# Kernel tuning notes

Hardware: AMD Instinct MI355X
Metric: run time of the kernel (lower is better)

The kernel has to match this reference:

```python
import jax, jax.numpy as jnp
import numpy as np

N_NODES = 50000
N_EDGES = 800000
N_FEAT = 128
HIDDEN = 128
N_CLASSES = 10
N_GRAPHS = 100


def setup_inputs() -> dict:
    key = jax.random.key(0)
    ks = jax.random.split(key, 16)
    x = jax.random.normal(ks[0], (N_NODES, N_FEAT), dtype=jnp.float32)
    edge_index = jax.random.randint(ks[1], (2, N_EDGES), 0, N_NODES, dtype=jnp.int64)
    batch = jnp.sort(jax.random.randint(ks[2], (N_NODES,), 0, N_GRAPHS, dtype=jnp.int64))

    def glorot(k, fi, fo):
        s = jnp.sqrt(6.0 / (fi + fo)).astype(jnp.float32)
        return jax.random.uniform(k, (fi, fo), jnp.float32, -s, s)

    return {
        "x": x,
        "edge_index": edge_index,
        "batch": batch,
        "W1": glorot(ks[3], N_FEAT, HIDDEN),
        "b1": jnp.zeros((HIDDEN,), jnp.float32),
        "W2": glorot(ks[4], HIDDEN, HIDDEN),
        "b2": jnp.zeros((HIDDEN,), jnp.float32),
        "W3": glorot(ks[5], HIDDEN, HIDDEN // 2),
        "b3": jnp.zeros((HIDDEN // 2,), jnp.float32),
        "Wf1": glorot(ks[6], HIDDEN // 2, 32),
        "bf1": jnp.zeros((32,), jnp.float32),
        "Wf2": glorot(ks[7], 32, N_CLASSES),
        "bf2": jnp.zeros((N_CLASSES,), jnp.float32),
    }


def _gcn_conv(x, row, col, norm, W, b, n_nodes):
    # GCNConv: x' = D^{-1/2}(A+I)D^{-1/2} (x W) + b
    h = x @ W                                            # [N, out]
    msg = h[row] * norm[:, None]                         # gather + scale per edge
    out = jax.ops.segment_sum(msg, col, num_segments=n_nodes)  # scatter-add to targets
    return out + b


def reference(x, edge_index, batch, W1, b1, W2, b2, W3, b3, Wf1, bf1, Wf2, bf2):
    n = x.shape[0]
    # add self-loops (PyG GCNConv default)
    loop = jnp.arange(n, dtype=edge_index.dtype)
    row = jnp.concatenate([edge_index[0], loop])
    col = jnp.concatenate([edge_index[1], loop])
    # symmetric normalization from in-degree at targets (edge_weight = 1)
    deg = jax.ops.segment_sum(jnp.ones_like(col, x.dtype), col, num_segments=n)
    dinv = jnp.where(deg > 0, jax.lax.rsqrt(deg), 0.0)
    norm = dinv[row] * dinv[col]                         # [E + N]

    h = jax.nn.relu(_gcn_conv(x, row, col, norm, W1, b1, n))
    h = jax.nn.relu(_gcn_conv(h, row, col, norm, W2, b2, n))
    h = jax.nn.relu(_gcn_conv(h, row, col, norm, W3, b3, n))

    # global_mean_pool over graphs
    sums = jax.ops.segment_sum(h, batch, num_segments=N_GRAPHS)
    cnts = jax.ops.segment_sum(jnp.ones((n,), h.dtype), batch, num_segments=N_GRAPHS)
    pooled = sums / jnp.maximum(cnts, 1.0)[:, None]      # [G, hidden//2]

    h = jax.nn.relu(pooled @ Wf1 + bf1)
    logits = h @ Wf2 + bf2                               # [G, num_classes]
    return logits
```

## Files before the change

### kernel.cpp

```cpp
#include <hip/hip_runtime.h>
#include <hip/hip_fp16.h>


#define NGRAPH 100
#define CAP 64

typedef _Float16 f16x8 __attribute__((ext_vector_type(8)));
typedef float f32x4 __attribute__((ext_vector_type(4)));


__global__ __launch_bounds__(256) void prep_all(const float* __restrict__ W1,
                                                const float* __restrict__ W2,
                                                const float* __restrict__ W3,
                                                __half* __restrict__ Wt1,
                                                __half* __restrict__ Wt2,
                                                __half* __restrict__ Wt3,
                                                int* __restrict__ cnt,
                                                float* __restrict__ pooled, int n) {
    const int idx = blockIdx.x * 256 + threadIdx.x;
    if (idx < 16384) {
        int nn = idx >> 7, k = idx & 127;
        Wt1[idx] = __float2half(W1[k * 128 + nn]);
    } else if (idx < 32768) {
        int j = idx - 16384;
        int nn = j >> 7, k = j & 127;
        Wt2[j] = __float2half(W2[k * 128 + nn]);
    } else if (idx < 40960) {
        int j = idx - 32768;
        int nn = j >> 7, k = j & 127;
        Wt3[j] = __float2half(W3[k * 64 + nn]);
    }
    if (idx < n) cnt[idx] = 0;
    if (idx < NGRAPH * 64) pooled[idx] = 0.0f;
}


__global__ void fill_bucket(const int* __restrict__ row, const int* __restrict__ col,
                            int* __restrict__ cnt, int* __restrict__ bucket,
                            int E, int colsPerGroup) {
    const int g  = blockIdx.x & 7;
    const int gb = blockIdx.x >> 3;
    const int nb = gridDim.x >> 3;
    const int lo = g * colsPerGroup, hi = lo + colsPerGroup;
    for (int e = gb * 256 + threadIdx.x; e < E; e += nb * 256) {
        int c = col[e];
        if (c >= lo && c < hi) {
            int pos = atomicAdd(&cnt[c], 1);
            bucket[c * CAP + pos] = row[e];
        }
    }
}


template <int OUT, bool F16IN>
__global__ __launch_bounds__(256) void gemm_mfma(const void* __restrict__ Xv,
                                                 const __half* __restrict__ Wt,
                                                 const float* __restrict__ bias_in,
                                                 const int* __restrict__ cnt,
                                                 __half* __restrict__ Yh, int n) {
    __shared__ _Float16 Xs[64 * 128];
    __shared__ _Float16 Ws[OUT * 128];
    __shared__ float bs[128];

    const float*  Xf = (const float*)Xv;
    const __half* Xh = (const __half*)Xv;

    const int t = threadIdx.x;
    if (t < 128) bs[t] = (bias_in != nullptr) ? bias_in[t] : 0.0f;
    __syncthreads();

    const int row0 = blockIdx.x * 64;
    const bool do_relu = (bias_in != nullptr);

    for (int c = t; c < 64 * 16; c += 256) {
        const int r = c >> 4, q = c & 15;
        const int gr = row0 + r;
        float vals[8];
        #pragma unroll
        for (int i = 0; i < 8; ++i) vals[i] = 0.0f;
        if (gr < n) {
            if (F16IN) {
                f16x8 hv = *(const f16x8*)&Xh[(size_t)gr * 128 + q * 8];
                #pragma unroll
                for (int i = 0; i < 8; ++i) vals[i] = (float)hv[i];
            } else {
                float4 va = *(const float4*)&Xf[(size_t)gr * 128 + q * 8];
                float4 vb = *(const float4*)&Xf[(size_t)gr * 128 + q * 8 + 4];
                vals[0] = va.x; vals[1] = va.y; vals[2] = va.z; vals[3] = va.w;
                vals[4] = vb.x; vals[5] = vb.y; vals[6] = vb.z; vals[7] = vb.w;
            }
        }
        if (do_relu) {
            const int k = q * 8;
            #pragma unroll
            for (int i = 0; i < 8; ++i) vals[i] = fmaxf(vals[i] + bs[k + i], 0.f);
        }
        f16x8 hv;
        #pragma unroll
        for (int i = 0; i < 8; ++i) hv[i] = (_Float16)vals[i];
        *(f16x8*)&Xs[(size_t)((r << 4) + (q ^ (r & 15))) * 8] = hv;
    }
    for (int c = t; c < OUT * 16; c += 256) {
        const int nn = c >> 4, q = c & 15;
        f16x8 w = *(const f16x8*)&Wt[nn * 128 + q * 8];
        *(f16x8*)&Ws[(size_t)((nn << 4) + (q ^ (nn & 15))) * 8] = w;
    }
    __syncthreads();

    constexpr int NT = OUT / 16;
    const int lane = t & 63, wave = t >> 6;
    const int m = lane & 15, quad = lane >> 4;

    f32x4 acc[NT];
    #pragma unroll
    for (int i = 0; i < NT; ++i) acc[i] = (f32x4){0.f, 0.f, 0.f, 0.f};

    #pragma unroll
    for (int s = 0; s < 4; ++s) {
        const int qa = s * 4 + quad;
        f16x8 a = *(const f16x8*)&Xs[(size_t)(((wave * 16 + m) << 4) + (qa ^ m)) * 8];
        #pragma unroll
        for (int tt = 0; tt < NT; ++tt) {
            f16x8 b = *(const f16x8*)&Ws[(size_t)(((tt * 16 + m) << 4) + (qa ^ m)) * 8];
            acc[tt] = __builtin_amdgcn_mfma_f32_16x16x32_f16(a, b, acc[tt], 0, 0, 0);
        }
    }

    #pragma unroll
    for (int i = 0; i < 4; ++i) {
        const int gr = row0 + wave * 16 + quad * 4 + i;
        if (gr < n) {
            const float dw = 1.0f / sqrtf((float)(cnt[gr] + 1));
            #pragma unroll
            for (int tt = 0; tt < NT; ++tt)
                Yh[(size_t)gr * OUT + tt * 16 + m] = __float2half(acc[tt][i] * dw);
        }
    }
}


template <int F>
__global__ void gather_kernel(const __half* __restrict__ hs, const int* __restrict__ cnt,
                              const int* __restrict__ bucket,
                              __half* __restrict__ outh, int n) {
    const int lane = threadIdx.x & 63;
    const int c = (blockIdx.x * blockDim.x + threadIdx.x) >> 6;
    if (c >= n) return;
    const int deg = cnt[c];
    const int beg = c * CAP;
    const int end = beg + deg;
    const int last = end - 1;
    const float w = 1.0f / sqrtf((float)(deg + 1));
    const float4* hq = (const float4*)hs;

    const int strm = lane >> 4;
    const int li   = lane & 15;

    float a[8];
    #pragma unroll
    for (int i = 0; i < 8; ++i) a[i] = 0.f;

    auto acc8 = [&](float4 raw, float m) {
        __half2 h0 = *(__half2*)&raw.x;
        __half2 h1 = *(__half2*)&raw.y;
        __half2 h2 = *(__half2*)&raw.z;
        __half2 h3 = *(__half2*)&raw.w;
        float2 f0 = __half22float2(h0), f1 = __half22float2(h1);
        float2 f2 = __half22float2(h2), f3 = __half22float2(h3);
        a[0] += m * f0.x; a[1] += m * f0.y;
        a[2] += m * f1.x; a[3] += m * f1.y;
        a[4] += m * f2.x; a[5] += m * f2.y;
        a[6] += m * f3.x; a[7] += m * f3.y;
    };

    if (strm == 0) acc8(hq[(size_t)c * 16 + li], 1.f);

    const int chunks = (deg + 15) >> 4;
    int j = beg + strm;
    for (int t = 0; t < chunks; ++t, j += 16) {
        const int j0 = j, j1 = j + 4, j2 = j + 8, j3 = j + 12;
        const int s0 = bucket[min(j0, last)];
        const int s1 = bucket[min(j1, last)];
        const int s2 = bucket[min(j2, last)];
        const int s3 = bucket[min(j3, last)];
        const float m0 = (j0 < end) ? 1.f : 0.f;
        const float m1 = (j1 < end) ? 1.f : 0.f;
        const float m2 = (j2 < end) ? 1.f : 0.f;
        const float m3 = (j3 < end) ? 1.f : 0.f;
        float4 v0 = hq[(size_t)s0 * 16 + li];
        float4 v1 = hq[(size_t)s1 * 16 + li];
        float4 v2 = hq[(size_t)s2 * 16 + li];
        float4 v3 = hq[(size_t)s3 * 16 + li];
        acc8(v0, m0);
        acc8(v1, m1);
        acc8(v2, m2);
        acc8(v3, m3);
    }

    #pragma unroll
    for (int i = 0; i < 8; ++i) {
        a[i] += __shfl(a[i], lane ^ 16);
        a[i] += __shfl(a[i], lane ^ 32);
    }
    if (strm == 0) {
        __half2 o0 = __float22half2_rn(make_float2(w * a[0], w * a[1]));
        __half2 o1 = __float22half2_rn(make_float2(w * a[2], w * a[3]));
        __half2 o2 = __float22half2_rn(make_float2(w * a[4], w * a[5]));
        __half2 o3 = __float22half2_rn(make_float2(w * a[6], w * a[7]));
        float4 o;
        o.x = *(float*)&o0;
        o.y = *(float*)&o1;
        o.z = *(float*)&o2;
        o.w = *(float*)&o3;
        *(float4*)&outh[(size_t)c * 128 + li * 8] = o;
    }
}


__global__ __launch_bounds__(256) void fused_gpool(const __half* __restrict__ hs,
                                                   const int* __restrict__ cnt,
                                                   const int* __restrict__ bucket,
                                                   const float* __restrict__ b3,
                                                   const int* __restrict__ batch,
                                                   float* __restrict__ pooled, int n) {
    const int lane  = threadIdx.x & 63;
    const int half  = lane >> 5;
    const int li    = lane & 31;
    const int wave  = (blockIdx.x * blockDim.x + threadIdx.x) >> 6;
    const int nwav  = (gridDim.x * blockDim.x) >> 6;
    const int chunk = (n + nwav - 1) / nwav;
    const int beg = wave * chunk;
    const int end = min(beg + chunk, n);
    if (beg >= end) return;
    const unsigned* h2 = (const unsigned*)hs;

    auto cvt2 = [](unsigned raw) { return __half22float2(*(__half2*)&raw); };

    const float bias0 = b3[li * 2], bias1 = b3[li * 2 + 1];
    int curg = batch[beg];
    float2 acc = make_float2(0.f, 0.f);
    for (int i = beg; i < end; ++i) {
        int g = batch[i];
        if (g != curg) {
            if (half == 0) {
                atomicAdd(&pooled[curg * 64 + li * 2],     acc.x);
                atomicAdd(&pooled[curg * 64 + li * 2 + 1], acc.y);
            }
            acc = make_float2(0.f, 0.f); curg = g;
        }
        const int deg = cnt[i];
        const float dv = 1.0f / sqrtf((float)(deg + 1));
        float2 sv = make_float2(0.f, 0.f);
        if (half == 0) sv = cvt2(h2[(size_t)i * 32 + li]);
        const int eb = i * CAP, ee = eb + deg;
        const int lastj = ee - 1;
        const int chks = (deg + 15) >> 4;
        int j = eb + half;
        for (int t = 0; t < chks; ++t, j += 16) {
            const int j0 = j,      j1 = j + 2,  j2 = j + 4,  j3 = j + 6;
            const int j4 = j + 8,  j5 = j + 10, j6 = j + 12, j7 = j + 14;
            const int a0 = bucket[min(j0, lastj)];
            const int a1 = bucket[min(j1, lastj)];
            const int a2 = bucket[min(j2, lastj)];
            const int a3 = bucket[min(j3, lastj)];
            const int a4 = bucket[min(j4, lastj)];
            const int a5 = bucket[min(j5, lastj)];
            const int a6 = bucket[min(j6, lastj)];
            const int a7 = bucket[min(j7, lastj)];
            const float m0 = (j0 < ee) ? 1.f : 0.f;
            const float m1 = (j1 < ee) ? 1.f : 0.f;
            const float m2 = (j2 < ee) ? 1.f : 0.f;
            const float m3 = (j3 < ee) ? 1.f : 0.f;
            const float m4 = (j4 < ee) ? 1.f : 0.f;
            const float m5 = (j5 < ee) ? 1.f : 0.f;
            const float m6 = (j6 < ee) ? 1.f : 0.f;
            const float m7 = (j7 < ee) ? 1.f : 0.f;
            float2 v0 = cvt2(h2[(size_t)a0 * 32 + li]);
            float2 v1 = cvt2(h2[(size_t)a1 * 32 + li]);
            float2 v2 = cvt2(h2[(size_t)a2 * 32 + li]);
            float2 v3 = cvt2(h2[(size_t)a3 * 32 + li]);
            float2 v4 = cvt2(h2[(size_t)a4 * 32 + li]);
            float2 v5 = cvt2(h2[(size_t)a5 * 32 + li]);
            float2 v6 = cvt2(h2[(size_t)a6 * 32 + li]);
            float2 v7 = cvt2(h2[(size_t)a7 * 32 + li]);
            sv.x += m0 * v0.x + m1 * v1.x + m2 * v2.x + m3 * v3.x
                  + m4 * v4.x + m5 * v5.x + m6 * v6.x + m7 * v7.x;
            sv.y += m0 * v0.y + m1 * v1.y + m2 * v2.y + m3 * v3.y
                  + m4 * v4.y + m5 * v5.y + m6 * v6.y + m7 * v7.y;
        }
        sv.x += __shfl(sv.x, lane ^ 32);
        sv.y += __shfl(sv.y, lane ^ 32);
        acc.x += fmaxf(dv * sv.x + bias0, 0.f);
        acc.y += fmaxf(dv * sv.y + bias1, 0.f);
    }
    if (half == 0) {
        atomicAdd(&pooled[curg * 64 + li * 2],     acc.x);
        atomicAdd(&pooled[curg * 64 + li * 2 + 1], acc.y);
    }
}


__global__ __launch_bounds__(64) void mlp_kernel(const float* __restrict__ pooled,
                                                 const int* __restrict__ batch,
                                                 const float* __restrict__ Wf1,
                                                 const float* __restrict__ bf1,
                                                 const float* __restrict__ Wf2,
                                                 const float* __restrict__ bf2,
                                                 float* __restrict__ out, int n) {
    const int g = blockIdx.x;
    const int t = threadIdx.x;

    auto lb = [&](int v) {
        int lo = 0, hi = n;
        while (lo < hi) { int mid = (lo + hi) >> 1; if (batch[mid] < v) lo = mid + 1; else hi = mid; }
        return lo;
    };
    const int cnt = lb(g + 1) - lb(g);

    __shared__ float pm[64];
    __shared__ float hid[32];

    pm[t] = pooled[g * 64 + t] / (float)(cnt > 0 ? cnt : 1);
    __syncthreads();

    if (t < 32) {
        float a = bf1[t];
        #pragma unroll
        for (int k = 0; k < 64; ++k) a += pm[k] * Wf1[k * 32 + t];
        hid[t] = fmaxf(a, 0.f);
    }
    __syncthreads();

    if (t < 10) {
        float a = bf2[t];
        #pragma unroll
        for (int k = 0; k < 32; ++k) a += hid[k] * Wf2[k * 10 + t];
        out[g * 10 + t] = a;
    }
}


extern "C" void kernel_launch(void* const* d_in, const int* in_sizes, int n_in,
                              void* d_out, int out_size, void* d_ws, size_t ws_size,
                              hipStream_t stream) {
    const float* x     = (const float*)d_in[0];
    const int*   edge  = (const int*)  d_in[1];
    const int*   batch = (const int*)  d_in[2];
    const float* W1    = (const float*)d_in[3];
    const float* b1    = (const float*)d_in[4];
    const float* W2    = (const float*)d_in[5];
    const float* b2    = (const float*)d_in[6];
    const float* W3    = (const float*)d_in[7];
    const float* b3    = (const float*)d_in[8];
    const float* Wf1   = (const float*)d_in[9];
    const float* bf1   = (const float*)d_in[10];
    const float* Wf2   = (const float*)d_in[11];
    const float* bf2   = (const float*)d_in[12];
    float* out = (float*)d_out;

    const int E = in_sizes[1] / 2;
    const int n = in_sizes[2];
    const int* row = edge;
    const int* col = edge + E;

    const int colsPerGroup = (n + 7) / 8;

    const size_t n_pad = ((size_t)n + 64) & ~(size_t)63;
    char* wsb = (char*)d_ws;
    int*    cnt    = (int*)wsb;                  wsb += n_pad * 4;
    float*  pooled = (float*)wsb;                wsb += NGRAPH * 64 * 4;
    int*    bucket = (int*)wsb;                  wsb += (size_t)n_pad * CAP * 4;
    __half* Wt1    = (__half*)wsb;               wsb += 16384 * 2;
    __half* Wt2    = (__half*)wsb;               wsb += 16384 * 2;
    __half* Wt3    = (__half*)wsb;               wsb += 8192 * 2;
    __half* bufA   = (__half*)wsb;               wsb += (size_t)n * 128 * 2;
    __half* bufB   = (__half*)wsb;

    prep_all<<<256, 256, 0, stream>>>(W1, W2, W3, Wt1, Wt2, Wt3, cnt, pooled, n);
    fill_bucket<<<1024, 256, 0, stream>>>(row, col, cnt, bucket, E, colsPerGroup);

    const int ggemm = (n + 63) / 64;
    const int gath_grid = (n * 64 + 255) / 256;

    gemm_mfma<128, false><<<ggemm, 256, 0, stream>>>(x, Wt1, nullptr, cnt, bufA, n);
    gather_kernel<128><<<gath_grid, 256, 0, stream>>>(bufA, cnt, bucket, bufB, n);
    gemm_mfma<128, true><<<ggemm, 256, 0, stream>>>(bufB, Wt2, b1, cnt, bufA, n);
    gather_kernel<128><<<gath_grid, 256, 0, stream>>>(bufA, cnt, bucket, bufB, n);
    gemm_mfma<64, true><<<ggemm, 256, 0, stream>>>(bufB, Wt3, b2, cnt, bufA, n);
    fused_gpool<<<2048, 256, 0, stream>>>(bufA, cnt, bucket, b3, batch, pooled, n);
    mlp_kernel<<<NGRAPH, 64, 0, stream>>>(pooled, batch, Wf1, bf1, Wf2, bf2, out, n);
}
```

Before: 259.5 us.

## Split fused layer-3 gather and pooling into per-node gather and separate pool kernel

The fused kernel that did the layer-3 neighbor gather, bias, ReLU and mean-pool accumulation is split in two. A per-node gather kernel (one wave per node, four streams of 16 lanes loading 8-byte half4 vectors) writes fp32 ReLU outputs to a buffer. A separate pool kernel then sums contiguous rows per graph with atomics. This spreads the irregular gather across many more waves for better latency hiding, at the cost of an extra kernel launch and an fp32 intermediate written to and read back from memory.

```diff
diff --git a/kernel.cpp b/kernel.cpp
--- a/kernel.cpp
+++ b/kernel.cpp
@@ -217,83 +217,106 @@
 }
 
 
-__global__ __launch_bounds__(256) void fused_gpool(const __half* __restrict__ hs,
-                                                   const int* __restrict__ cnt,
-                                                   const int* __restrict__ bucket,
-                                                   const float* __restrict__ b3,
+__global__ void gather_relu64(const __half* __restrict__ hs, const int* __restrict__ cnt,
+                              const int* __restrict__ bucket,
+                              const float* __restrict__ b3,
+                              float* __restrict__ fout, int n) {
+    const int lane = threadIdx.x & 63;
+    const int c = (blockIdx.x * blockDim.x + threadIdx.x) >> 6;
+    if (c >= n) return;
+    const int deg = cnt[c];
+    const int beg = c * CAP;
+    const int end = beg + deg;
+    const int last = end - 1;
+    const float dv = 1.0f / sqrtf((float)(deg + 1));
+    const float2* hq = (const float2*)hs;
+
+    const int strm = lane >> 4;
+    const int li   = lane & 15;
+
+    float a[4] = {0.f, 0.f, 0.f, 0.f};
+
+    auto acc4 = [&](float2 raw, float m) {
+        __half2 ha = *(__half2*)&raw.x;
+        __half2 hb = *(__half2*)&raw.y;
+        float2 fa = __half22float2(ha);
+        float2 fb = __half22float2(hb);
+        a[0] += m * fa.x; a[1] += m * fa.y;
+        a[2] += m * fb.x; a[3] += m * fb.y;
+    };
+
+    if (strm == 0) acc4(hq[(size_t)c * 16 + li], 1.f);
+
+    const int chunks = (deg + 15) >> 4;
+    int j = beg + strm;
+    for (int t = 0; t < chunks; ++t, j += 16) {
+        const int j0 = j, j1 = j + 4, j2 = j + 8, j3 = j + 12;
+        const int s0 = bucket[min(j0, last)];
+        const int s1 = bucket[min(j1, last)];
+        const int s2 = bucket[min(j2, last)];
+        const int s3 = bucket[min(j3, last)];
+        const float m0 = (j0 < end) ? 1.f : 0.f;
+        const float m1 = (j1 < end) ? 1.f : 0.f;
+        const float m2 = (j2 < end) ? 1.f : 0.f;
+        const float m3 = (j3 < end) ? 1.f : 0.f;
+        float2 v0 = hq[(size_t)s0 * 16 + li];
+        float2 v1 = hq[(size_t)s1 * 16 + li];
+        float2 v2 = hq[(size_t)s2 * 16 + li];
+        float2 v3 = hq[(size_t)s3 * 16 + li];
+        acc4(v0, m0);
+        acc4(v1, m1);
+        acc4(v2, m2);
+        acc4(v3, m3);
+    }
+
+    #pragma unroll
+    for (int i = 0; i < 4; ++i) {
+        a[i] += __shfl(a[i], lane ^ 16);
+        a[i] += __shfl(a[i], lane ^ 32);
+    }
+    if (strm == 0) {
+        float4 bb = *(const float4*)&b3[li * 4];
+        float4 o;
+        o.x = fmaxf(dv * a[0] + bb.x, 0.f);
+        o.y = fmaxf(dv * a[1] + bb.y, 0.f);
+        o.z = fmaxf(dv * a[2] + bb.z, 0.f);
+        o.w = fmaxf(dv * a[3] + bb.w, 0.f);
+        *(float4*)&fout[(size_t)c * 64 + li * 4] = o;
+    }
+}
+
+
+__global__ __launch_bounds__(256) void pool_kernel(const float* __restrict__ fout,
                                                    const int* __restrict__ batch,
                                                    float* __restrict__ pooled, int n) {
-    const int lane  = threadIdx.x & 63;
-    const int half  = lane >> 5;
-    const int li    = lane & 31;
-    const int wave  = (blockIdx.x * blockDim.x + threadIdx.x) >> 6;
-    const int nwav  = (gridDim.x * blockDim.x) >> 6;
+    const int lane = threadIdx.x & 63;
+    const int half = lane >> 5;
+    const int li   = lane & 31;
+    const int wave = (blockIdx.x * blockDim.x + threadIdx.x) >> 6;
+    const int nwav = (gridDim.x * blockDim.x) >> 6;
     const int chunk = (n + nwav - 1) / nwav;
     const int beg = wave * chunk;
     const int end = min(beg + chunk, n);
     if (beg >= end) return;
-    const unsigned* h2 = (const unsigned*)hs;
-
-    auto cvt2 = [](unsigned raw) { return __half22float2(*(__half2*)&raw); };
-
-    const float bias0 = b3[li * 2], bias1 = b3[li * 2 + 1];
-    int curg = batch[beg];
+    const float2* pf = (const float2*)fout;
+
+    int curg = -1;
     float2 acc = make_float2(0.f, 0.f);
-    for (int i = beg; i < end; ++i) {
-        int g = batch[i];
+    for (int i = beg + half; i < end; i += 2) {
+        const int g = batch[i];
         if (g != curg) {
-            if (half == 0) {
+            if (curg >= 0) {
                 atomicAdd(&pooled[curg * 64 + li * 2],     acc.x);
                 atomicAdd(&pooled[curg * 64 + li * 2 + 1], acc.y);
             }
-            acc = make_float2(0.f, 0.f); curg = g;
-        }
-        const int deg = cnt[i];
-        const float dv = 1.0f / sqrtf((float)(deg + 1));
-        float2 sv = make_float2(0.f, 0.f);
-        if (half == 0) sv = cvt2(h2[(size_t)i * 32 + li]);
-        const int eb = i * CAP, ee = eb + deg;
-        const int lastj = ee - 1;
-        const int chks = (deg + 15) >> 4;
-        int j = eb + half;
-        for (int t = 0; t < chks; ++t, j += 16) {
-            const int j0 = j,      j1 = j + 2,  j2 = j + 4,  j3 = j + 6;
-            const int j4 = j + 8,  j5 = j + 10, j6 = j + 12, j7 = j + 14;
-            const int a0 = bucket[min(j0, lastj)];
-            const int a1 = bucket[min(j1, lastj)];
-            const int a2 = bucket[min(j2, lastj)];
-            const int a3 = bucket[min(j3, lastj)];
-            const int a4 = bucket[min(j4, lastj)];
-            const int a5 = bucket[min(j5, lastj)];
-            const int a6 = bucket[min(j6, lastj)];
-            const int a7 = bucket[min(j7, lastj)];
-            const float m0 = (j0 < ee) ? 1.f : 0.f;
-            const float m1 = (j1 < ee) ? 1.f : 0.f;
-            const float m2 = (j2 < ee) ? 1.f : 0.f;
-            const float m3 = (j3 < ee) ? 1.f : 0.f;
-            const float m4 = (j4 < ee) ? 1.f : 0.f;
-            const float m5 = (j5 < ee) ? 1.f : 0.f;
-            const float m6 = (j6 < ee) ? 1.f : 0.f;
-            const float m7 = (j7 < ee) ? 1.f : 0.f;
-            float2 v0 = cvt2(h2[(size_t)a0 * 32 + li]);
-            float2 v1 = cvt2(h2[(size_t)a1 * 32 + li]);
-            float2 v2 = cvt2(h2[(size_t)a2 * 32 + li]);
-            float2 v3 = cvt2(h2[(size_t)a3 * 32 + li]);
-            float2 v4 = cvt2(h2[(size_t)a4 * 32 + li]);
-            float2 v5 = cvt2(h2[(size_t)a5 * 32 + li]);
-            float2 v6 = cvt2(h2[(size_t)a6 * 32 + li]);
-            float2 v7 = cvt2(h2[(size_t)a7 * 32 + li]);
-            sv.x += m0 * v0.x + m1 * v1.x + m2 * v2.x + m3 * v3.x
-                  + m4 * v4.x + m5 * v5.x + m6 * v6.x + m7 * v7.x;
-            sv.y += m0 * v0.y + m1 * v1.y + m2 * v2.y + m3 * v3.y
-                  + m4 * v4.y + m5 * v5.y + m6 * v6.y + m7 * v7.y;
-        }
-        sv.x += __shfl(sv.x, lane ^ 32);
-        sv.y += __shfl(sv.y, lane ^ 32);
-        acc.x += fmaxf(dv * sv.x + bias0, 0.f);
-        acc.y += fmaxf(dv * sv.y + bias1, 0.f);
-    }
-    if (half == 0) {
+            acc = make_float2(0.f, 0.f);
+            curg = g;
+        }
+        float2 v = pf[(size_t)i * 32 + li];
+        acc.x += v.x;
+        acc.y += v.y;
+    }
+    if (curg >= 0) {
         atomicAdd(&pooled[curg * 64 + li * 2],     acc.x);
         atomicAdd(&pooled[curg * 64 + li * 2 + 1], acc.y);
     }
@@ -387,6 +410,7 @@
     gemm_mfma<128, true><<<ggemm, 256, 0, stream>>>(bufB, Wt2, b1, cnt, bufA, n);
     gather_kernel<128><<<gath_grid, 256, 0, stream>>>(bufA, cnt, bucket, bufB, n);
     gemm_mfma<64, true><<<ggemm, 256, 0, stream>>>(bufB, Wt3, b2, cnt, bufA, n);
-    fused_gpool<<<2048, 256, 0, stream>>>(bufA, cnt, bucket, b3, batch, pooled, n);
+    gather_relu64<<<gath_grid, 256, 0, stream>>>(bufA, cnt, bucket, b3, (float*)bufB, n);
+    pool_kernel<<<2048, 256, 0, stream>>>((const float*)bufB, batch, pooled, n);
     mlp_kernel<<<NGRAPH, 64, 0, stream>>>(pooled, batch, Wf1, bf1, Wf2, bf2, out, n);
 }
```

Result: slower. 283.0 us (+9.1%).
